# Kernel tuning notes

Hardware: AMD Instinct MI355X
Metric: run time of the kernel (lower is better)

Reference implementation:

```python
import jax, jax.numpy as jnp
import numpy as np

# Model dims: nSet=48, nItemMax=80, input feat=512,
# D = baseChn*max_channel_ratio = 128 = head_size, H = num_heads = 2.
S, N, DIN = 48, 80, 512
D = 128
H, HS = 2, 128
EPS = 1e-3  # layer_normalization epsilon (non-set-norm branch)

def _w(key, fi, fo):
    return jax.random.normal(key, (fi, fo), jnp.float32) / np.sqrt(fi)

def setup_inputs() -> dict:
    key = jax.random.key(0)
    ks = jax.random.split(key, 20)
    sizes = jax.random.randint(ks[0], (S,), 1, N + 1)
    x = jax.random.normal(ks[1], (S, N, DIN), jnp.float32)
    item_mask = (jnp.arange(N)[None, :] < sizes[:, None]).astype(jnp.float32)
    x = x * item_mask[:, :, None]  # zero-pad invalid items (drives ==0 masks)
    return {
        "x": x,
        "x_size": sizes.astype(jnp.float32),
        # trainable MLP (fc1/fc2/fc3, gelu, no bias)
        "W1": _w(ks[2], DIN, 512),
        "W2": _w(ks[3], 512, 256),
        "W3": _w(ks[4], 256, D),
        # encoder self-attention layer
        "Wq_s": _w(ks[5], D, H * HS),
        "Wk_s": _w(ks[6], D, H * HS),
        "Wv_s": _w(ks[7], D, H * HS),
        "Wh_s": _w(ks[8], H * HS, HS),
        "Wfc_e": _w(ks[9], D, D),
        # decoder cross-set attention layer
        "Wq_c": _w(ks[10], D, H * HS),
        "Wk_c": _w(ks[11], D, H * HS),
        "Wv_c": _w(ks[12], D, H * HS),
        "Wh_c": _w(ks[13], H * HS, HS),
        "Wfc_d": _w(ks[14], D, D),
        # cross_set_score
        "Wcs": _w(ks[15], D, H * HS),
        "Wcs2": _w(ks[16], H, 1),
    }

def _gelu(z):
    return jax.nn.gelu(z, approximate=False)  # tf.nn.gelu default

def _item_norm(x):
    # layer_normalization with is_set_norm=False: per-item LN, zero padded rows
    mean = jnp.mean(x, axis=-1, keepdims=True)
    std = jnp.std(x, axis=-1, keepdims=True)
    norm = (x - mean) / (std + EPS)
    keep = jnp.sum(x, axis=-1, keepdims=True) != 0
    return jnp.where(keep, norm, jnp.zeros_like(x))

def _masked_softmax(s):
    # faithful to source: mask entries where raw score == 0
    m = s != 0
    e = jnp.where(m, jnp.exp(s - jnp.max(s, axis=-1, keepdims=True)), 0.0)
    return e / (jnp.sum(e, axis=-1, keepdims=True) + 1e-10)

def _mha(q_in, kv_in, Wq, Wk, Wv, Wh):
    # q_in/kv_in: [S, S, N, D]
    q = (q_in @ Wq).reshape(S, S, N, H, HS)
    k = (kv_in @ Wk).reshape(S, S, N, H, HS)
    v = (kv_in @ Wv).reshape(S, S, N, H, HS)
    s = jnp.einsum('xynhd,xymhd->xyhnm', q, k) / np.sqrt(HS)
    a = _masked_softmax(s)
    o = jnp.einsum('xyhnm,xymhd->xynhd', a, v).reshape(S, S, N, H * HS)
    return o @ Wh  # -> [S, S, N, HS]

def reference(x, x_size, W1, W2, W3, Wq_s, Wk_s, Wv_s, Wh_s, Wfc_e,
              Wq_c, Wk_c, Wv_c, Wh_c, Wfc_d, Wcs, Wcs2):
    # item-wise MLP projection: feat -> 512 -> 256 -> 128
    h = _gelu(_gelu(_gelu(x @ W1) @ W2) @ W3)  # [S, N, D]
    # pairwise set grid [nSet_x, nSet_y, nItemMax, D]
    x4 = jnp.broadcast_to(h[:, None], (S, S, N, D))
    # encoder: self-attention over items within each (i,j) pair
    z = _item_norm(x4)
    x4 = x4 + _mha(z, z, Wq_s, Wk_s, Wv_s, Wh_s)
    z = _item_norm(x4)
    x4 = x4 + _gelu(z @ Wfc_e)
    # decoder: cross-set attention, out[i,j] = Attn(q=z[i,j], kv=z[j,i])
    z = _item_norm(x4)
    x4 = x4 + _mha(z, jnp.transpose(z, (1, 0, 2, 3)), Wq_c, Wk_c, Wv_c, Wh_c)
    z = _item_norm(x4)
    x4 = x4 + _gelu(z @ Wfc_d)
    # cross_set_score: pairwise ReLU-matmul, set-size normalized
    xh = (x4 @ Wcs).reshape(S, S, N, H, HS).transpose(0, 1, 3, 2, 4)  # [j,i,h,n,d]
    A = jax.nn.relu(jnp.einsum('jihnd,ijhmd->jihnm', xh, xh) / np.sqrt(HS))
    sc = A.sum((-1, -2)) / x_size[None, :, None] / x_size[:, None, None]  # [S,S,H]
    return sc @ Wcs2  # [S, S, 1]
```

## Files before the change

### kernel.cpp

```cpp
#include <hip/hip_runtime.h>
#include <hip/hip_bf16.h>


#define SS 48
#define NI 80

typedef unsigned short us;
typedef __attribute__((ext_vector_type(8))) short s8v;
typedef __attribute__((ext_vector_type(4))) float f4v;

#define MFMA(a,b,c) __builtin_amdgcn_mfma_f32_16x16x32_bf16((a),(b),(c),0,0,0)

__device__ __forceinline__ float gelu_f(float x){
  return 0.5f * x * (1.0f + erff(x * 0.7071067811865475f));
}
__device__ __forceinline__ us f2b(float f){
  __hip_bfloat16 b = __float2bfloat16(f);
  return reinterpret_cast<us&>(b);
}
__device__ __forceinline__ s8v zero8(){ s8v v = {0,0,0,0,0,0,0,0}; return v; }
__device__ __forceinline__ void gl16(const void* g, void* l){
  __builtin_amdgcn_global_load_lds(
      (const __attribute__((address_space(1))) void*)g,
      (__attribute__((address_space(3))) void*)l, 16, 0, 0);
}

template<int ABF16, int OUTF32>
__global__ __launch_bounds__(256) void mgemm_k(const void* __restrict__ Ap,
    const float* __restrict__ B, void* __restrict__ Cp, int N, int K)
{
  __shared__ __align__(16) char lds[10240];
  char* As = lds; char* Bs = lds + 5120;
  const int t = threadIdx.x;
  const int wv = t >> 6, lm = t & 15, lh = (t >> 4) & 3;
  const int bx = blockIdx.x, by = blockIdx.y;
  const int ar = wv*16 + lm, r0 = wv*16 + lh*4;
  f4v acc[4];
#pragma unroll
  for (int ct = 0; ct < 4; ++ct) acc[ct] = {0.f,0.f,0.f,0.f};
  const int rA = t >> 2, kcA = (t & 3) << 3;
  const int kkB = t >> 3, nnB = (t & 7) << 3;
  for (int k0 = 0; k0 < K; k0 += 32) {
    __syncthreads();
    if (ABF16) {
      s8v v = *(const s8v*)((const us*)Ap + (size_t)(by*64 + rA)*K + k0 + kcA);
      *(s8v*)(As + rA*80 + kcA*2) = v;
    } else {
      const float* ap = (const float*)Ap + (size_t)(by*64 + rA)*K + k0 + kcA;
      float4 v0 = *(const float4*)ap, v1 = *(const float4*)(ap + 4);
      us tmp[8] = {f2b(v0.x),f2b(v0.y),f2b(v0.z),f2b(v0.w),
                   f2b(v1.x),f2b(v1.y),f2b(v1.z),f2b(v1.w)};
      *(s8v*)(As + rA*80 + kcA*2) = *(const s8v*)tmp;
    }
    {
      const float* bp = B + (size_t)(k0 + kkB)*N + bx*64 + nnB;
      float4 w0 = *(const float4*)bp, w1 = *(const float4*)(bp + 4);
      float w8[8] = {w0.x,w0.y,w0.z,w0.w,w1.x,w1.y,w1.z,w1.w};
#pragma unroll
      for (int q = 0; q < 8; ++q)
        *(us*)(Bs + (nnB + q)*80 + kkB*2) = f2b(w8[q]);
    }
    __syncthreads();
    s8v af = *(const s8v*)(As + ar*80 + lh*16);
#pragma unroll
    for (int ct = 0; ct < 4; ++ct) {
      s8v bf = *(const s8v*)(Bs + (ct*16 + lm)*80 + lh*16);
      acc[ct] = MFMA(af, bf, acc[ct]);
    }
  }
#pragma unroll
  for (int ct = 0; ct < 4; ++ct)
#pragma unroll
    for (int reg = 0; reg < 4; ++reg) {
      size_t r = by*64 + r0 + reg;
      int c = bx*64 + ct*16 + lm;
      float v = gelu_f(acc[ct][reg]);
      if (OUTF32) ((float*)Cp)[r*N + c] = v;
      else ((us*)Cp)[r*N + c] = f2b(v);
    }
}

__global__ __launch_bounds__(256) void qkv_k(const us* __restrict__ A,
    const float* __restrict__ Wq, const float* __restrict__ Wk,
    const float* __restrict__ Wv, us* __restrict__ Qb, us* __restrict__ Kb,
    us* __restrict__ VT)
{
  __shared__ __align__(16) char lds[10240];
  char* As = lds; char* Bs = lds + 5120;
  const int t = threadIdx.x;
  const int wv = t >> 6, lm = t & 15, lh = (t >> 4) & 3;
  const int bx = blockIdx.x, by = blockIdx.y;
  const int sel = bx >> 2, bxx = bx & 3;
  const float* B = sel == 0 ? Wq : (sel == 1 ? Wk : Wv);
  const int ar = wv*16 + lm, r0 = wv*16 + lh*4;
  f4v acc[4];
#pragma unroll
  for (int ct = 0; ct < 4; ++ct) acc[ct] = {0.f,0.f,0.f,0.f};
  const int rA = t >> 2, kcA = (t & 3) << 3;
  const int kkB = t >> 3, nnB = (t & 7) << 3;
#pragma unroll
  for (int k0 = 0; k0 < 128; k0 += 32) {
    __syncthreads();
    {
      s8v v = *(const s8v*)(A + (size_t)(by*64 + rA)*128 + k0 + kcA);
      *(s8v*)(As + rA*80 + kcA*2) = v;
      const float* bp = B + (size_t)(k0 + kkB)*256 + bxx*64 + nnB;
      float4 w0 = *(const float4*)bp, w1 = *(const float4*)(bp + 4);
      float w8[8] = {w0.x,w0.y,w0.z,w0.w,w1.x,w1.y,w1.z,w1.w};
#pragma unroll
      for (int q = 0; q < 8; ++q)
        *(us*)(Bs + (nnB + q)*80 + kkB*2) = f2b(w8[q]);
    }
    __syncthreads();
    s8v af = *(const s8v*)(As + ar*80 + lh*16);
#pragma unroll
    for (int ct = 0; ct < 4; ++ct) {
      s8v bf = *(const s8v*)(Bs + (ct*16 + lm)*80 + lh*16);
      acc[ct] = MFMA(af, bf, acc[ct]);
    }
  }
  if (sel < 2) {
    us* O = sel ? Kb : Qb;
#pragma unroll
    for (int ct = 0; ct < 4; ++ct)
#pragma unroll
      for (int reg = 0; reg < 4; ++reg)
        O[(size_t)(by*64 + r0 + reg)*256 + bxx*64 + ct*16 + lm] = f2b(acc[ct][reg]);
  } else {
#pragma unroll
    for (int ct = 0; ct < 4; ++ct)
#pragma unroll
      for (int reg = 0; reg < 4; ++reg) {
        int r = by*64 + r0 + reg;
        int s = r / 80, m = r % 80;
        int d = bxx*64 + ct*16 + lm;
        VT[((size_t)s*256 + d)*80 + m] = f2b(acc[ct][reg]);
      }
  }
}

__global__ __launch_bounds__(64) void norm_k(const float* __restrict__ in,
                                             us* __restrict__ out)
{
  const int r = blockIdx.x, t = threadIdx.x;
  float v0 = in[(size_t)r*128 + t];
  float v1 = in[(size_t)r*128 + t + 64];
  float sm = v0 + v1;
#pragma unroll
  for (int off = 1; off < 64; off <<= 1) sm += __shfl_xor(sm, off, 64);
  float mean = sm * (1.0f/128.0f);
  float d0 = v0 - mean, d1 = v1 - mean;
  float vs = d0*d0 + d1*d1;
#pragma unroll
  for (int off = 1; off < 64; off <<= 1) vs += __shfl_xor(vs, off, 64);
  float inv = 1.0f / (sqrtf(vs * (1.0f/128.0f)) + 1e-3f);
  bool keep = (sm != 0.0f);
  out[(size_t)r*128 + t]      = f2b(keep ? d0*inv : 0.0f);
  out[(size_t)r*128 + t + 64] = f2b(keep ? d1*inv : 0.0f);
}

__global__ __launch_bounds__(128) void prep_k(
    const float* __restrict__ Wh_s, const float* __restrict__ Wfc_e,
    const float* __restrict__ Wh_c, const float* __restrict__ Wfc_d,
    const float* __restrict__ Wcs,  const float* __restrict__ Wv_s,
    const float* __restrict__ Wv_c,
    us* __restrict__ WfcTe, us* __restrict__ WfcTd,
    float* __restrict__ Wvh_s, float* __restrict__ Wvh_c,
    us* __restrict__ Mb)
{
  const int x = blockIdx.x, task = blockIdx.y, tid = threadIdx.x;
  if (task == 0) {
    WfcTe[x*128 + tid] = f2b(Wfc_e[(size_t)tid*128 + x]);
  } else if (task == 1) {
    WfcTd[x*128 + tid] = f2b(Wfc_d[(size_t)tid*128 + x]);
  } else if (task < 6) {
    int h = (task - 2) & 1;
    const float* Wv = task < 4 ? Wv_s : Wv_c;
    const float* Wh = task < 4 ? Wh_s : Wh_c;
    float* Wvh = task < 4 ? Wvh_s : Wvh_c;
    float acc = 0.f;
#pragma unroll 8
    for (int d = 0; d < 128; ++d)
      acc = fmaf(Wv[(size_t)x*256 + h*128 + d], Wh[(size_t)(h*128 + d)*128 + tid], acc);
    Wvh[(size_t)x*256 + h*128 + tid] = acc;
  } else {
    int h = task - 6;
    float acc = 0.f;
#pragma unroll 8
    for (int k = 0; k < 128; ++k)
      acc = fmaf(Wcs[(size_t)x*256 + h*128 + k], Wcs[(size_t)tid*256 + h*128 + k], acc);
    Mb[(size_t)h*16384 + x*128 + tid] = f2b(acc);
  }
}

__device__ __forceinline__ void attn4e(int a, int t,
    const us* __restrict__ Qg, const us* __restrict__ Kg,
    const us* __restrict__ VTg, const float* __restrict__ baseg,
    const us* __restrict__ WfcT,
    char* __restrict__ X, char* __restrict__ Y, f4v x4[8])
{
  const int wv = t >> 6, lane = t & 63, lm = t & 15, lh = (t >> 4) & 3;
  const int ar = wv*16 + lm, r0 = wv*16 + lh*4;
  const float isq = 0.08838834764831845f;
  const int b = a;
#pragma unroll
  for (int dt = 0; dt < 8; ++dt) x4[dt] = (f4v){0.f,0.f,0.f,0.f};

#pragma unroll 1
  for (int h = 0; h < 2; ++h) {
    if (h == 1) __syncthreads();
#pragma unroll
    for (int c = 0; c < 4; ++c) {
      int chunk = wv*4 + c;
      int row = chunk*4 + (lane >> 4);
      int scb = ((lane & 15) << 4) ^ ((row & 7) << 4);
      gl16(Kg + (((size_t)(b*NI + row)) << 8) + h*128 + (scb >> 1), X + chunk*1024);
    }
    s8v qf[4];
    {
      const us* qrow = Qg + (((size_t)(a*NI + ar)) << 8) + h*128 + lh*8;
#pragma unroll
      for (int ks = 0; ks < 4; ++ks) qf[ks] = *(const s8v*)(qrow + ks*32);
    }
    __syncthreads();
    f4v sA[5];
#pragma unroll
    for (int nt = 0; nt < 5; ++nt) {
      int row = nt*16 + lm;
      f4v acc = (f4v){0.f,0.f,0.f,0.f};
#pragma unroll
      for (int ks = 0; ks < 4; ++ks) {
        s8v kf = *(const s8v*)(X + row*256 + ((ks*64 + lh*16) ^ ((row & 7) << 4)));
        acc = MFMA(qf[ks], kf, acc);
      }
      sA[nt] = acc;
    }
#pragma unroll
    for (int reg = 0; reg < 4; ++reg) {
      int r = r0 + reg;
      float sv[5];
#pragma unroll
      for (int nt = 0; nt < 5; ++nt) sv[nt] = sA[nt][reg] * isq;
      float mx = sv[0];
#pragma unroll
      for (int nt = 1; nt < 5; ++nt) mx = fmaxf(mx, sv[nt]);
#pragma unroll
      for (int off = 1; off < 16; off <<= 1) mx = fmaxf(mx, __shfl_xor(mx, off, 64));
      float e[5], sum = 0.f;
#pragma unroll
      for (int nt = 0; nt < 5; ++nt) {
        e[nt] = (sv[nt] != 0.f) ? __expf(sv[nt] - mx) : 0.f;
        sum += e[nt];
      }
#pragma unroll
      for (int off = 1; off < 16; off <<= 1) sum += __shfl_xor(sum, off, 64);
      float inv = 1.f / (sum + 1e-10f);
#pragma unroll
      for (int nt = 0; nt < 5; ++nt)
        *(us*)(Y + r*256 + ((2*(nt*16 + lm)) ^ ((r & 7) << 4))) = f2b(e[nt] * inv);
    }
    s8v pf0 = *(const s8v*)(Y + ar*256 + ((lh*16) ^ ((ar & 7) << 4)));
    s8v pf1 = *(const s8v*)(Y + ar*256 + ((64 + lh*16) ^ ((ar & 7) << 4)));
    s8v pf2 = zero8();
    if (lh < 2)
      pf2 = *(const s8v*)(Y + ar*256 + ((128 + lh*16) ^ ((ar & 7) << 4)));
    __syncthreads();
#pragma unroll
    for (int c = 0; c < 4; ++c) {
      int chunk = wv*4 + c;
      int L = chunk*1024 + lane*16;
      int rv = L / 160;
      int rem = L - rv*160;
      int cv = (rem >> 4) - (rv % 10); if (cv < 0) cv += 10;
      gl16(VTg + ((size_t)(b*256 + h*128 + rv))*80 + (cv << 3), X + chunk*1024);
    }
    __syncthreads();
#pragma unroll
    for (int dt = 0; dt < 8; ++dt) {
      int row = dt*16 + lm;
      int rm = (row % 10) << 4;
      int o0 = lh*16 + rm; if (o0 >= 160) o0 -= 160;
      x4[dt] = MFMA(pf0, *(const s8v*)(X + row*160 + o0), x4[dt]);
      int o1 = 64 + lh*16 + rm; if (o1 >= 160) o1 -= 160;
      x4[dt] = MFMA(pf1, *(const s8v*)(X + row*160 + o1), x4[dt]);
      s8v v2 = zero8();
      if (lh < 2) {
        int o2 = 128 + lh*16 + rm; if (o2 >= 160) o2 -= 160;
        v2 = *(const s8v*)(X + row*160 + o2);
      }
      x4[dt] = MFMA(pf2, v2, x4[dt]);
    }
    if (h == 1) {
#pragma unroll
      for (int reg = 0; reg < 4; ++reg) {
        int r = r0 + reg;
#pragma unroll
        for (int dt = 0; dt < 8; ++dt)
          x4[dt][reg] += baseg[(((size_t)(a*NI + r)) << 7) + dt*16 + lm];
      }
    }
  }

  __syncthreads();
  for (int chunk = wv; chunk < 16; chunk += 5) {
    int row = chunk*4 + (lane >> 4);
    int scb = ((lane & 15) << 4) ^ ((row & 7) << 4);
    gl16(WfcT + (size_t)row*128 + (scb >> 1), X + chunk*1024);
  }
#pragma unroll
  for (int reg = 0; reg < 4; ++reg) {
    int r = r0 + reg;
    float sm = 0.f;
#pragma unroll
    for (int dt = 0; dt < 8; ++dt) sm += x4[dt][reg];
#pragma unroll
    for (int off = 1; off < 16; off <<= 1) sm += __shfl_xor(sm, off, 64);
    float mean = sm * (1.0f/128.0f);
    float vs = 0.f;
#pragma unroll
    for (int dt = 0; dt < 8; ++dt) { float d = x4[dt][reg] - mean; vs = fmaf(d, d, vs); }
#pragma unroll
    for (int off = 1; off < 16; off <<= 1) vs += __shfl_xor(vs, off, 64);
    float inv = 1.f / (sqrtf(vs * (1.0f/128.0f)) + 1e-3f);
    bool keep = (sm != 0.f);
#pragma unroll
    for (int dt = 0; dt < 8; ++dt)
      *(us*)(Y + r*256 + ((2*(dt*16 + lm)) ^ ((r & 7) << 4))) = f2b(keep ? (x4[dt][reg]-mean)*inv : 0.f);
  }
  s8v zf[4];
#pragma unroll
  for (int ks = 0; ks < 4; ++ks)
    zf[ks] = *(const s8v*)(Y + ar*256 + ((ks*64 + lh*16) ^ ((ar & 7) << 4)));
  __syncthreads();
#pragma unroll
  for (int dt = 0; dt < 4; ++dt) {
    int row = dt*16 + lm;
    f4v acc = (f4v){0.f,0.f,0.f,0.f};
#pragma unroll
    for (int ks = 0; ks < 4; ++ks) {
      s8v wfr = *(const s8v*)(X + row*256 + ((ks*64 + lh*16) ^ ((row & 7) << 4)));
      acc = MFMA(zf[ks], wfr, acc);
    }
#pragma unroll
    for (int reg = 0; reg < 4; ++reg) x4[dt][reg] += gelu_f(acc[reg]);
  }
  __syncthreads();
  for (int chunk = wv; chunk < 16; chunk += 5) {
    int row = chunk*4 + (lane >> 4);
    int scb = ((lane & 15) << 4) ^ ((row & 7) << 4);
    gl16(WfcT + (size_t)(row + 64)*128 + (scb >> 1), X + chunk*1024);
  }
  __syncthreads();
#pragma unroll
  for (int dt = 4; dt < 8; ++dt) {
    int row = dt*16 + lm;
    int r2 = row - 64;
    f4v acc = (f4v){0.f,0.f,0.f,0.f};
#pragma unroll
    for (int ks = 0; ks < 4; ++ks) {
      s8v wfr = *(const s8v*)(X + r2*256 + ((ks*64 + lh*16) ^ ((row & 7) << 4)));
      acc = MFMA(zf[ks], wfr, acc);
    }
#pragma unroll
    for (int reg = 0; reg < 4; ++reg) x4[dt][reg] += gelu_f(acc[reg]);
  }
}

__global__ __launch_bounds__(320) void enc_k(
    const us* __restrict__ Qg, const us* __restrict__ Kg,
    const us* __restrict__ VTg, const float* __restrict__ hb,
    const us* __restrict__ WfcT, float* __restrict__ e2p,
    us* __restrict__ z3b)
{
  __shared__ __align__(16) char X[20480];
  __shared__ __align__(16) char Y[20480];
  const int t = threadIdx.x;
  const int wv = t >> 6, lm = t & 15, lh = (t >> 4) & 3;
  const int r0 = wv*16 + lh*4;
  const int i = blockIdx.x;
  f4v x4[8];
  attn4e(i, t, Qg, Kg, VTg, hb, WfcT, X, Y, x4);
#pragma unroll
  for (int reg = 0; reg < 4; ++reg) {
    int r = r0 + reg;
    size_t gb = ((size_t)(i*NI + r)) << 7;
    float tmp[8]; float sm = 0.f;
#pragma unroll
    for (int dt = 0; dt < 8; ++dt) { tmp[dt] = x4[dt][reg]; sm += tmp[dt]; }
    *(float4*)(e2p + gb + lm*8)     = make_float4(tmp[0],tmp[1],tmp[2],tmp[3]);
    *(float4*)(e2p + gb + lm*8 + 4) = make_float4(tmp[4],tmp[5],tmp[6],tmp[7]);
#pragma unroll
    for (int off = 1; off < 16; off <<= 1) sm += __shfl_xor(sm, off, 64);
    float mean = sm * (1.0f/128.0f);
    float vs = 0.f;
#pragma unroll
    for (int dt = 0; dt < 8; ++dt) { float d = tmp[dt] - mean; vs = fmaf(d, d, vs); }
#pragma unroll
    for (int off = 1; off < 16; off <<= 1) vs += __shfl_xor(vs, off, 64);
    float inv = 1.f / (sqrtf(vs * (1.0f/128.0f)) + 1e-3f);
    bool keep = (sm != 0.f);
#pragma unroll
    for (int dt = 0; dt < 8; ++dt)
      z3b[gb + dt*16 + lm] = f2b(keep ? (tmp[dt]-mean)*inv : 0.f);
  }
}

__global__ __launch_bounds__(640, 2) void dec8_k(
    const us* __restrict__ Qg, const us* __restrict__ Kg,
    const us* __restrict__ VTg, const float* __restrict__ e2p,
    const us* __restrict__ WfcT, us* __restrict__ x4g)
{
  __shared__ __align__(16) char L[155648];
  const int t = threadIdx.x;
  const int g = (t >= 320) ? 1 : 0;
  const int tg = t - g*320;
  const int wv = tg >> 6, wb = t >> 6;
  const int lane = t & 63, lm = t & 15, lh = (t >> 4) & 3;
  const int ar = wv*16 + lm, r0 = wv*16 + lh*4;
  const float isq = 0.08838834764831845f;
  const int a = blockIdx.x, b = blockIdx.y*2 + g;
  char* W  = L;
  char* S0 = L + 32768 + g*61440;
  char* S1 = S0 + 20480;
  char* Y  = S0 + 40960;

#define STG_K(DST, H)                                                        \
  { _Pragma("unroll") for (int c_ = 0; c_ < 4; ++c_) {                       \
      int ch_ = wv*4 + c_;                                                   \
      int rw_ = ch_*4 + (lane >> 4);                                         \
      int sc_ = ((lane & 15) << 4) ^ ((rw_ & 7) << 4);                       \
      gl16(Kg + (((size_t)(b*NI + rw_)) << 8) + (H)*128 + (sc_ >> 1),        \
           (DST) + ch_*1024); } }
#define STG_VT(DST, H)                                                       \
  { _Pragma("unroll") for (int c_ = 0; c_ < 4; ++c_) {                       \
      int ch_ = wv*4 + c_;                                                   \
      int L_ = ch_*1024 + lane*16;                                           \
      int rv_ = L_ / 160;                                                    \
      int cv_ = ((L_ - rv_*160) >> 4) - (rv_ % 10); if (cv_ < 0) cv_ += 10;  \
      gl16(VTg + ((size_t)(b*256 + (H)*128 + rv_))*80 + (cv_ << 3),          \
           (DST) + ch_*1024); } }
#define QKSM(KS, H)                                                          \
  { s8v qf_[4];                                                              \
    { const us* qr_ = Qg + (((size_t)(a*NI + ar)) << 8) + (H)*128 + lh*8;    \
      _Pragma("unroll") for (int ks = 0; ks < 4; ++ks)                       \
        qf_[ks] = *(const s8v*)(qr_ + ks*32); }                              \
    f4v sA_[5];                                                              \
    _Pragma("unroll") for (int nt = 0; nt < 5; ++nt) {                       \
      int rw_ = nt*16 + lm;                                                  \
      f4v ac_ = (f4v){0.f,0.f,0.f,0.f};                                      \
      _Pragma("unroll") for (int ks = 0; ks < 4; ++ks) {                     \
        s8v kf_ = *(const s8v*)((KS) + rw_*256 +                             \
                                ((ks*64 + lh*16) ^ ((rw_ & 7) << 4)));       \
        ac_ = MFMA(qf_[ks], kf_, ac_); }                                     \
      sA_[nt] = ac_; }                                                       \
    _Pragma("unroll") for (int reg = 0; reg < 4; ++reg) {                    \
      int r_ = r0 + reg;                                                     \
      float sv_[5];                                                          \
      _Pragma("unroll") for (int nt = 0; nt < 5; ++nt)                       \
        sv_[nt] = sA_[nt][reg] * isq;                                        \
      float mx_ = sv_[0];                                                    \
      _Pragma("unroll") for (int nt = 1; nt < 5; ++nt)                       \
        mx_ = fmaxf(mx_, sv_[nt]);                                           \
      _Pragma("unroll") for (int of_ = 1; of_ < 16; of_ <<= 1)               \
        mx_ = fmaxf(mx_, __shfl_xor(mx_, of_, 64));                          \
      float e_[5], su_ = 0.f;                                                \
      _Pragma("unroll") for (int nt = 0; nt < 5; ++nt) {                     \
        e_[nt] = (sv_[nt] != 0.f) ? __expf(sv_[nt] - mx_) : 0.f;             \
        su_ += e_[nt]; }                                                     \
      _Pragma("unroll") for (int of_ = 1; of_ < 16; of_ <<= 1)               \
        su_ += __shfl_xor(su_, of_, 64);                                     \
      float iv_ = 1.f / (su_ + 1e-10f);                                      \
      _Pragma("unroll") for (int nt = 0; nt < 5; ++nt)                       \
        *(us*)(Y + r_*256 + ((2*(nt*16 + lm)) ^ ((r_ & 7) << 4))) =          \
            f2b(e_[nt] * iv_); } }
#define PV(VS)                                                               \
  { s8v pf0_ = *(const s8v*)(Y + ar*256 + ((lh*16) ^ ((ar & 7) << 4)));      \
    s8v pf1_ = *(const s8v*)(Y + ar*256 + ((64 + lh*16) ^ ((ar & 7) << 4))); \
    s8v pf2_ = zero8();                                                      \
    if (lh < 2)                                                              \
      pf2_ = *(const s8v*)(Y + ar*256 + ((128 + lh*16) ^ ((ar & 7) << 4)));  \
    _Pragma("unroll") for (int dt = 0; dt < 8; ++dt) {                       \
      int rw_ = dt*16 + lm;                                                  \
      int rm_ = (rw_ % 10) << 4;                                             \
      int o0_ = lh*16 + rm_; if (o0_ >= 160) o0_ -= 160;                     \
      x4[dt] = MFMA(pf0_, *(const s8v*)((VS) + rw_*160 + o0_), x4[dt]);      \
      int o1_ = 64 + lh*16 + rm_; if (o1_ >= 160) o1_ -= 160;                \
      x4[dt] = MFMA(pf1_, *(const s8v*)((VS) + rw_*160 + o1_), x4[dt]);      \
      s8v v2_ = zero8();                                                     \
      if (lh < 2) { int o2_ = 128 + lh*16 + rm_;                             \
        if (o2_ >= 160) o2_ -= 160;                                          \
        v2_ = *(const s8v*)((VS) + rw_*160 + o2_); }                         \
      x4[dt] = MFMA(pf2_, v2_, x4[dt]); } }

  f4v x4[8];
#pragma unroll
  for (int dt = 0; dt < 8; ++dt) x4[dt] = (f4v){0.f,0.f,0.f,0.f};

  for (int ch = wb; ch < 32; ch += 10) {
    int row = ch*4 + (lane >> 4);
    int scb = ((lane & 15) << 4) ^ ((row & 7) << 4);
    gl16(WfcT + (size_t)row*128 + (scb >> 1), W + ch*1024);
  }
  STG_K(S0, 0);
  __syncthreads();
  STG_VT(S1, 0);
  QKSM(S0, 0);
  __syncthreads();
  STG_K(S0, 1);
  PV(S1);
  __syncthreads();
  STG_VT(S1, 1);
  QKSM(S0, 1);
  __syncthreads();
  PV(S1);
#pragma unroll
  for (int reg = 0; reg < 4; ++reg) {
    const f4v* bp = (const f4v*)(e2p + (((size_t)(a*NI + r0 + reg)) << 7) + lm*8);
    f4v bb0 = bp[0], bb1 = bp[1];
#pragma unroll
    for (int dt = 0; dt < 4; ++dt) {
      x4[dt][reg]   += bb0[dt];
      x4[dt+4][reg] += bb1[dt];
    }
  }
#pragma unroll
  for (int reg = 0; reg < 4; ++reg) {
    int r = r0 + reg;
    float sm = 0.f;
#pragma unroll
    for (int dt = 0; dt < 8; ++dt) sm += x4[dt][reg];
#pragma unroll
    for (int off = 1; off < 16; off <<= 1) sm += __shfl_xor(sm, off, 64);
    float mean = sm * (1.0f/128.0f);
    float vs = 0.f;
#pragma unroll
    for (int dt = 0; dt < 8; ++dt) { float d = x4[dt][reg] - mean; vs = fmaf(d, d, vs); }
#pragma unroll
    for (int off = 1; off < 16; off <<= 1) vs += __shfl_xor(vs, off, 64);
    float inv = 1.f / (sqrtf(vs * (1.0f/128.0f)) + 1e-3f);
    bool keep = (sm != 0.f);
#pragma unroll
    for (int dt = 0; dt < 8; ++dt)
      *(us*)(Y + r*256 + ((2*(dt*16 + lm)) ^ ((r & 7) << 4))) = f2b(keep ? (x4[dt][reg]-mean)*inv : 0.f);
  }
  {
    s8v zf[4];
#pragma unroll
    for (int ks = 0; ks < 4; ++ks)
      zf[ks] = *(const s8v*)(Y + ar*256 + ((ks*64 + lh*16) ^ ((ar & 7) << 4)));
#pragma unroll
    for (int dt = 0; dt < 8; ++dt) {
      int row = dt*16 + lm;
      f4v ac = (f4v){0.f,0.f,0.f,0.f};
#pragma unroll
      for (int ks = 0; ks < 4; ++ks) {
        s8v wf = *(const s8v*)(W + row*256 + ((ks*64 + lh*16) ^ ((row & 7) << 4)));
        ac = MFMA(zf[ks], wf, ac);
      }
#pragma unroll
      for (int reg = 0; reg < 4; ++reg) x4[dt][reg] += gelu_f(ac[reg]);
    }
  }
#pragma unroll
  for (int reg = 0; reg < 4; ++reg) {
    int r = r0 + reg;
#pragma unroll
    for (int dt = 0; dt < 8; ++dt)
      *(us*)(Y + r*256 + ((2*(dt*16 + lm)) ^ ((r & 7) << 4))) = f2b(x4[dt][reg]);
  }
  {
    char* dst = (char*)(x4g + ((size_t)a*SS + b)*10240);
#pragma unroll
    for (int q = 0; q < 4; ++q) {
      int c = lane + q*64;
      int row = wv*16 + (c >> 4);
      int cb = (c & 15) << 4;
      s8v v = *(const s8v*)(Y + row*256 + (cb ^ ((row & 7) << 4)));
      *(s8v*)(dst + row*256 + cb) = v;
    }
  }
#undef STG_K
#undef STG_VT
#undef QKSM
#undef PV
}

__global__ __launch_bounds__(320) void up_k(
    const us* __restrict__ x4g, const us* __restrict__ Mb,
    const float* __restrict__ Wcs2, const float* __restrict__ xsg,
    float* __restrict__ outg)
{
  __shared__ __align__(16) char As[20480];
  __shared__ __align__(16) char Bs[16384];
  __shared__ __align__(16) char Xi[20480];
  __shared__ __align__(16) char Xu[40960];
  __shared__ float red[10];
  const int t = threadIdx.x;
  const int wv = t >> 6, lane = t & 63, lm = t & 15, lh = (t >> 4) & 3;
  const int ar = wv*16 + lm, r0 = wv*16 + lh*4;
  const float isq = 0.08838834764831845f;

  int bid0 = blockIdx.x;
  int bid = (bid0 & 7) * 147 + (bid0 >> 3);
  int ii = (int)(0.5f*(97.0f - sqrtf(9409.0f - 8.0f*(float)bid)));
  if (ii > 47) ii = 47; if (ii < 0) ii = 0;
  while (ii*SS - ii*(ii-1)/2 > bid) --ii;
  while ((ii+1)*SS - (ii+1)*ii/2 <= bid) ++ii;
  const int i = ii, j = ii + (bid - (ii*SS - ii*(ii-1)/2));
  const us* Aji = x4g + ((size_t)j*SS + i)*10240;
  const us* Aij = x4g + ((size_t)i*SS + j)*10240;

#pragma unroll
  for (int c = 0; c < 4; ++c) {
    int chunk = wv*4 + c;
    int row = chunk*4 + (lane >> 4);
    int scb = ((lane & 15) << 4) ^ ((row & 7) << 4);
    gl16(Aji + (size_t)row*128 + (scb >> 1), As + chunk*1024);
    gl16(Aij + (size_t)row*128 + (scb >> 1), Xi + chunk*1024);
  }
  f4v acc[16];
#pragma unroll
  for (int ct = 0; ct < 16; ++ct) acc[ct] = (f4v){0.f,0.f,0.f,0.f};
#pragma unroll 1
  for (int k0 = 0; k0 < 128; k0 += 32) {
    if (k0) __syncthreads();
    for (int c = wv; c < 16; c += 5) {
      int row = c*16 + (lane >> 2);
      int colb = (lane & 3) << 4;
      int scb = colb ^ ((row & 3) << 4);
      gl16(Mb + (size_t)row*128 + k0 + (scb >> 1), Bs + c*1024);
    }
    __syncthreads();
    int ks = k0 >> 5;
    s8v af = *(const s8v*)(As + ar*256 + ((ks*64 + lh*16) ^ ((ar & 7) << 4)));
#pragma unroll
    for (int ct = 0; ct < 16; ++ct) {
      int row = ct*16 + lm;
      s8v bf = *(const s8v*)(Bs + row*64 + ((lh*16) ^ ((row & 3) << 4)));
      acc[ct] = MFMA(af, bf, acc[ct]);
    }
  }
#pragma unroll
  for (int ct = 0; ct < 16; ++ct) {
    int h = ct >> 3;
    int cl = (ct & 7)*16 + lm;
#pragma unroll
    for (int reg = 0; reg < 4; ++reg) {
      int row = r0 + reg;
      *(us*)(Xu + h*20480 + row*256 + ((2*cl) ^ ((row & 7) << 4))) = f2b(acc[ct][reg]);
    }
  }
  __syncthreads();
  s8v xf[4];
#pragma unroll
  for (int ks = 0; ks < 4; ++ks)
    xf[ks] = *(const s8v*)(Xi + ar*256 + ((ks*64 + lh*16) ^ ((ar & 7) << 4)));
  float sc[2];
#pragma unroll 1
  for (int h = 0; h < 2; ++h) {
    const char* Xh = Xu + h*20480;
    float loc = 0.f;
#pragma unroll
    for (int nt = 0; nt < 5; ++nt) {
      int brow = nt*16 + lm;
      f4v ac = (f4v){0.f,0.f,0.f,0.f};
#pragma unroll
      for (int ks = 0; ks < 4; ++ks) {
        s8v bf = *(const s8v*)(Xh + brow*256 + ((ks*64 + lh*16) ^ ((brow & 7) << 4)));
        ac = MFMA(xf[ks], bf, ac);
      }
#pragma unroll
      for (int reg = 0; reg < 4; ++reg) loc += fmaxf(ac[reg]*isq, 0.f);
    }
    sc[h] = loc;
  }
#pragma unroll
  for (int off = 1; off < 64; off <<= 1) {
    sc[0] += __shfl_xor(sc[0], off, 64);
    sc[1] += __shfl_xor(sc[1], off, 64);
  }
  if ((t & 63) == 0) { red[wv] = sc[0]; red[wv + 5] = sc[1]; }
  __syncthreads();
  if (t == 0) {
    float s0 = red[0]+red[1]+red[2]+red[3]+red[4];
    float s1 = red[5]+red[6]+red[7]+red[8]+red[9];
    float val = (s0*Wcs2[0] + s1*Wcs2[1]) / (xsg[i]*xsg[j]);
    outg[i*SS + j] = val;
    outg[j*SS + i] = val;
  }
}

extern "C" void kernel_launch(void* const* d_in, const int* in_sizes, int n_in,
                              void* d_out, int out_size, void* d_ws, size_t ws_size,
                              hipStream_t stream)
{
  (void)in_sizes; (void)n_in; (void)out_size; (void)ws_size;
  const float* x     = (const float*)d_in[0];
  const float* xs    = (const float*)d_in[1];
  const float* W1    = (const float*)d_in[2];
  const float* W2    = (const float*)d_in[3];
  const float* W3    = (const float*)d_in[4];
  const float* Wq_s  = (const float*)d_in[5];
  const float* Wk_s  = (const float*)d_in[6];
  const float* Wv_s  = (const float*)d_in[7];
  const float* Wh_s  = (const float*)d_in[8];
  const float* Wfc_e = (const float*)d_in[9];
  const float* Wq_c  = (const float*)d_in[10];
  const float* Wk_c  = (const float*)d_in[11];
  const float* Wv_c  = (const float*)d_in[12];
  const float* Wh_c  = (const float*)d_in[13];
  const float* Wfc_d = (const float*)d_in[14];
  const float* Wcs   = (const float*)d_in[15];
  const float* Wcs2  = (const float*)d_in[16];
  float* out = (float*)d_out;

  char* w = (char*)d_ws;
  us* h1b     = (us*)w;    w += (size_t)3840*512*2;
  us* h2b     = (us*)w;    w += (size_t)3840*256*2;
  float* hb   = (float*)w; w += (size_t)3840*128*4;
  us* zb16    = (us*)w;    w += (size_t)3840*128*2;
  us* z3b     = (us*)w;    w += (size_t)3840*128*2;
  float* e2p  = (float*)w; w += (size_t)3840*128*4;
  us* Qb      = (us*)w;    w += (size_t)3840*256*2;
  us* Kb      = (us*)w;    w += (size_t)3840*256*2;
  us* VT      = (us*)w;    w += (size_t)48*256*80*2;
  us* WfcTe   = (us*)w;    w += 16384*2;
  us* WfcTd   = (us*)w;    w += 16384*2;
  us* Mb      = (us*)w;    w += 32768*2;
  float* Wvh_s = (float*)w; w += 32768*4;
  float* Wvh_c = (float*)w; w += 32768*4;
  us* x4g     = (us*)w;    w += (size_t)2304*10240*2;

  hipLaunchKernelGGL(prep_k, dim3(128, 8), dim3(128), 0, stream,
                     Wh_s, Wfc_e, Wh_c, Wfc_d, Wcs, Wv_s, Wv_c,
                     WfcTe, WfcTd, Wvh_s, Wvh_c, Mb);
  hipLaunchKernelGGL((mgemm_k<0,0>), dim3(8,60), dim3(256), 0, stream,
                     (const void*)x, W1, (void*)h1b, 512, 512);
  hipLaunchKernelGGL((mgemm_k<1,0>), dim3(4,60), dim3(256), 0, stream,
                     (const void*)h1b, W2, (void*)h2b, 256, 512);
  hipLaunchKernelGGL((mgemm_k<1,1>), dim3(2,60), dim3(256), 0, stream,
                     (const void*)h2b, W3, (void*)hb, 128, 256);
  hipLaunchKernelGGL(norm_k, dim3(3840), dim3(64), 0, stream, hb, zb16);
  hipLaunchKernelGGL(qkv_k, dim3(12,60), dim3(256), 0, stream,
                     zb16, Wq_s, Wk_s, Wvh_s, Qb, Kb, VT);
  hipLaunchKernelGGL(enc_k, dim3(48), dim3(320), 0, stream,
                     Qb, Kb, VT, hb, WfcTe, e2p, z3b);
  hipLaunchKernelGGL(qkv_k, dim3(12,60), dim3(256), 0, stream,
                     z3b, Wq_c, Wk_c, Wvh_c, Qb, Kb, VT);
  hipLaunchKernelGGL(dec8_k, dim3(48,24), dim3(640), 0, stream,
                     Qb, Kb, VT, e2p, WfcTd, x4g);
  hipLaunchKernelGGL(up_k, dim3(1176), dim3(320), 0, stream,
                     x4g, Mb, Wcs2, xs, out);
}
```

Before: 239.9 us.

## Pre-convert inputs and weights to bf16 and fuse W3 GEMM with item norm

A single conversion kernel casts x and the MLP and Q/K weights to bf16 up front, so the GEMM kernels load bf16 directly instead of converting fp32 per tile. The third MLP GEMM now computes all 128 columns per block and fuses the GELU plus per-item layer norm, removing the separate norm kernel and its launch. Wvh is stored as bf16 and the base-add in attention uses vectorized loads. The extra conversion pass adds a full read and write of x (about 3840x512 elements) plus an extra launch, which may offset the savings.

Result: no change. 243.9 us (+1.7%).

```diff
diff --git a/kernel.cpp b/kernel.cpp
--- a/kernel.cpp
+++ b/kernel.cpp
@@ -25,138 +25,29 @@
       (__attribute__((address_space(3))) void*)l, 16, 0, 0);
 }
 
-template<int ABF16, int OUTF32>
-__global__ __launch_bounds__(256) void mgemm_k(const void* __restrict__ Ap,
-    const float* __restrict__ B, void* __restrict__ Cp, int N, int K)
-{
-  __shared__ __align__(16) char lds[10240];
-  char* As = lds; char* Bs = lds + 5120;
-  const int t = threadIdx.x;
-  const int wv = t >> 6, lm = t & 15, lh = (t >> 4) & 3;
-  const int bx = blockIdx.x, by = blockIdx.y;
-  const int ar = wv*16 + lm, r0 = wv*16 + lh*4;
-  f4v acc[4];
-#pragma unroll
-  for (int ct = 0; ct < 4; ++ct) acc[ct] = {0.f,0.f,0.f,0.f};
-  const int rA = t >> 2, kcA = (t & 3) << 3;
-  const int kkB = t >> 3, nnB = (t & 7) << 3;
-  for (int k0 = 0; k0 < K; k0 += 32) {
-    __syncthreads();
-    if (ABF16) {
-      s8v v = *(const s8v*)((const us*)Ap + (size_t)(by*64 + rA)*K + k0 + kcA);
-      *(s8v*)(As + rA*80 + kcA*2) = v;
-    } else {
-      const float* ap = (const float*)Ap + (size_t)(by*64 + rA)*K + k0 + kcA;
-      float4 v0 = *(const float4*)ap, v1 = *(const float4*)(ap + 4);
-      us tmp[8] = {f2b(v0.x),f2b(v0.y),f2b(v0.z),f2b(v0.w),
-                   f2b(v1.x),f2b(v1.y),f2b(v1.z),f2b(v1.w)};
-      *(s8v*)(As + rA*80 + kcA*2) = *(const s8v*)tmp;
-    }
-    {
-      const float* bp = B + (size_t)(k0 + kkB)*N + bx*64 + nnB;
-      float4 w0 = *(const float4*)bp, w1 = *(const float4*)(bp + 4);
-      float w8[8] = {w0.x,w0.y,w0.z,w0.w,w1.x,w1.y,w1.z,w1.w};
-#pragma unroll
-      for (int q = 0; q < 8; ++q)
-        *(us*)(Bs + (nnB + q)*80 + kkB*2) = f2b(w8[q]);
-    }
-    __syncthreads();
-    s8v af = *(const s8v*)(As + ar*80 + lh*16);
-#pragma unroll
-    for (int ct = 0; ct < 4; ++ct) {
-      s8v bf = *(const s8v*)(Bs + (ct*16 + lm)*80 + lh*16);
-      acc[ct] = MFMA(af, bf, acc[ct]);
-    }
-  }
-#pragma unroll
-  for (int ct = 0; ct < 4; ++ct)
-#pragma unroll
-    for (int reg = 0; reg < 4; ++reg) {
-      size_t r = by*64 + r0 + reg;
-      int c = bx*64 + ct*16 + lm;
-      float v = gelu_f(acc[ct][reg]);
-      if (OUTF32) ((float*)Cp)[r*N + c] = v;
-      else ((us*)Cp)[r*N + c] = f2b(v);
-    }
-}
-
-__global__ __launch_bounds__(256) void qkv_k(const us* __restrict__ A,
-    const float* __restrict__ Wq, const float* __restrict__ Wk,
-    const float* __restrict__ Wv, us* __restrict__ Qb, us* __restrict__ Kb,
-    us* __restrict__ VT)
-{
-  __shared__ __align__(16) char lds[10240];
-  char* As = lds; char* Bs = lds + 5120;
-  const int t = threadIdx.x;
-  const int wv = t >> 6, lm = t & 15, lh = (t >> 4) & 3;
-  const int bx = blockIdx.x, by = blockIdx.y;
-  const int sel = bx >> 2, bxx = bx & 3;
-  const float* B = sel == 0 ? Wq : (sel == 1 ? Wk : Wv);
-  const int ar = wv*16 + lm, r0 = wv*16 + lh*4;
-  f4v acc[4];
-#pragma unroll
-  for (int ct = 0; ct < 4; ++ct) acc[ct] = {0.f,0.f,0.f,0.f};
-  const int rA = t >> 2, kcA = (t & 3) << 3;
-  const int kkB = t >> 3, nnB = (t & 7) << 3;
-#pragma unroll
-  for (int k0 = 0; k0 < 128; k0 += 32) {
-    __syncthreads();
-    {
-      s8v v = *(const s8v*)(A + (size_t)(by*64 + rA)*128 + k0 + kcA);
-      *(s8v*)(As + rA*80 + kcA*2) = v;
-      const float* bp = B + (size_t)(k0 + kkB)*256 + bxx*64 + nnB;
-      float4 w0 = *(const float4*)bp, w1 = *(const float4*)(bp + 4);
-      float w8[8] = {w0.x,w0.y,w0.z,w0.w,w1.x,w1.y,w1.z,w1.w};
-#pragma unroll
-      for (int q = 0; q < 8; ++q)
-        *(us*)(Bs + (nnB + q)*80 + kkB*2) = f2b(w8[q]);
-    }
-    __syncthreads();
-    s8v af = *(const s8v*)(As + ar*80 + lh*16);
-#pragma unroll
-    for (int ct = 0; ct < 4; ++ct) {
-      s8v bf = *(const s8v*)(Bs + (ct*16 + lm)*80 + lh*16);
-      acc[ct] = MFMA(af, bf, acc[ct]);
-    }
-  }
-  if (sel < 2) {
-    us* O = sel ? Kb : Qb;
-#pragma unroll
-    for (int ct = 0; ct < 4; ++ct)
-#pragma unroll
-      for (int reg = 0; reg < 4; ++reg)
-        O[(size_t)(by*64 + r0 + reg)*256 + bxx*64 + ct*16 + lm] = f2b(acc[ct][reg]);
-  } else {
-#pragma unroll
-    for (int ct = 0; ct < 4; ++ct)
-#pragma unroll
-      for (int reg = 0; reg < 4; ++reg) {
-        int r = by*64 + r0 + reg;
-        int s = r / 80, m = r % 80;
-        int d = bxx*64 + ct*16 + lm;
-        VT[((size_t)s*256 + d)*80 + m] = f2b(acc[ct][reg]);
-      }
-  }
-}
-
-__global__ __launch_bounds__(64) void norm_k(const float* __restrict__ in,
-                                             us* __restrict__ out)
-{
-  const int r = blockIdx.x, t = threadIdx.x;
-  float v0 = in[(size_t)r*128 + t];
-  float v1 = in[(size_t)r*128 + t + 64];
-  float sm = v0 + v1;
-#pragma unroll
-  for (int off = 1; off < 64; off <<= 1) sm += __shfl_xor(sm, off, 64);
-  float mean = sm * (1.0f/128.0f);
-  float d0 = v0 - mean, d1 = v1 - mean;
-  float vs = d0*d0 + d1*d1;
-#pragma unroll
-  for (int off = 1; off < 64; off <<= 1) vs += __shfl_xor(vs, off, 64);
-  float inv = 1.0f / (sqrtf(vs * (1.0f/128.0f)) + 1e-3f);
-  bool keep = (sm != 0.0f);
-  out[(size_t)r*128 + t]      = f2b(keep ? d0*inv : 0.0f);
-  out[(size_t)r*128 + t + 64] = f2b(keep ? d1*inv : 0.0f);
+__global__ __launch_bounds__(256) void cvt_k(
+    const float* __restrict__ x,    const float* __restrict__ W1,
+    const float* __restrict__ W2,   const float* __restrict__ W3,
+    const float* __restrict__ Wq_s, const float* __restrict__ Wk_s,
+    const float* __restrict__ Wq_c, const float* __restrict__ Wk_c,
+    us* __restrict__ xb,   us* __restrict__ W1b, us* __restrict__ W2b,
+    us* __restrict__ W3b,  us* __restrict__ Wqsb, us* __restrict__ Wksb,
+    us* __restrict__ Wqcb, us* __restrict__ Wkcb)
+{
+  const int NX = 1966080;
+  const int C1 = NX + 262144, C2 = C1 + 131072, C3 = C2 + 32768;
+  const int C4 = C3 + 32768, C5 = C4 + 32768, C6 = C5 + 32768, C7 = C6 + 32768;
+  for (int idx = blockIdx.x*256 + threadIdx.x; idx < C7;
+       idx += gridDim.x*256) {
+    if (idx < NX)      xb[idx]        = f2b(x[idx]);
+    else if (idx < C1) W1b[idx - NX]  = f2b(W1[idx - NX]);
+    else if (idx < C2) W2b[idx - C1]  = f2b(W2[idx - C1]);
+    else if (idx < C3) W3b[idx - C2]  = f2b(W3[idx - C2]);
+    else if (idx < C4) Wqsb[idx - C3] = f2b(Wq_s[idx - C3]);
+    else if (idx < C5) Wksb[idx - C4] = f2b(Wk_s[idx - C4]);
+    else if (idx < C6) Wqcb[idx - C5] = f2b(Wq_c[idx - C5]);
+    else               Wkcb[idx - C6] = f2b(Wk_c[idx - C6]);
+  }
 }
 
 __global__ __launch_bounds__(128) void prep_k(
@@ -165,7 +56,7 @@
     const float* __restrict__ Wcs,  const float* __restrict__ Wv_s,
     const float* __restrict__ Wv_c,
     us* __restrict__ WfcTe, us* __restrict__ WfcTd,
-    float* __restrict__ Wvh_s, float* __restrict__ Wvh_c,
+    us* __restrict__ Wvhb_s, us* __restrict__ Wvhb_c,
     us* __restrict__ Mb)
 {
   const int x = blockIdx.x, task = blockIdx.y, tid = threadIdx.x;
@@ -177,12 +68,12 @@
     int h = (task - 2) & 1;
     const float* Wv = task < 4 ? Wv_s : Wv_c;
     const float* Wh = task < 4 ? Wh_s : Wh_c;
-    float* Wvh = task < 4 ? Wvh_s : Wvh_c;
+    us* Wvh = task < 4 ? Wvhb_s : Wvhb_c;
     float acc = 0.f;
 #pragma unroll 8
     for (int d = 0; d < 128; ++d)
       acc = fmaf(Wv[(size_t)x*256 + h*128 + d], Wh[(size_t)(h*128 + d)*128 + tid], acc);
-    Wvh[(size_t)x*256 + h*128 + tid] = acc;
+    Wvh[(size_t)x*256 + h*128 + tid] = f2b(acc);
   } else {
     int h = task - 6;
     float acc = 0.f;
@@ -190,6 +81,166 @@
     for (int k = 0; k < 128; ++k)
       acc = fmaf(Wcs[(size_t)x*256 + h*128 + k], Wcs[(size_t)tid*256 + h*128 + k], acc);
     Mb[(size_t)h*16384 + x*128 + tid] = f2b(acc);
+  }
+}
+
+__global__ __launch_bounds__(256) void bgemm_k(const us* __restrict__ A,
+    const us* __restrict__ B, us* __restrict__ C, int N, int K)
+{
+  __shared__ __align__(16) char lds[10240];
+  char* As = lds; char* Bs = lds + 5120;
+  const int t = threadIdx.x;
+  const int wv = t >> 6, lm = t & 15, lh = (t >> 4) & 3;
+  const int bx = blockIdx.x, by = blockIdx.y;
+  const int ar = wv*16 + lm, r0 = wv*16 + lh*4;
+  f4v acc[4];
+#pragma unroll
+  for (int ct = 0; ct < 4; ++ct) acc[ct] = {0.f,0.f,0.f,0.f};
+  const int rA = t >> 2, kcA = (t & 3) << 3;
+  const int kkB = t >> 3, nnB = (t & 7) << 3;
+  for (int k0 = 0; k0 < K; k0 += 32) {
+    __syncthreads();
+    {
+      s8v v = *(const s8v*)(A + (size_t)(by*64 + rA)*K + k0 + kcA);
+      *(s8v*)(As + rA*80 + kcA*2) = v;
+      s8v wv8 = *(const s8v*)(B + (size_t)(k0 + kkB)*N + bx*64 + nnB);
+      const us* wp = (const us*)&wv8;
+#pragma unroll
+      for (int q = 0; q < 8; ++q)
+        *(us*)(Bs + (nnB + q)*80 + kkB*2) = wp[q];
+    }
+    __syncthreads();
+    s8v af = *(const s8v*)(As + ar*80 + lh*16);
+#pragma unroll
+    for (int ct = 0; ct < 4; ++ct) {
+      s8v bf = *(const s8v*)(Bs + (ct*16 + lm)*80 + lh*16);
+      acc[ct] = MFMA(af, bf, acc[ct]);
+    }
+  }
+#pragma unroll
+  for (int ct = 0; ct < 4; ++ct)
+#pragma unroll
+    for (int reg = 0; reg < 4; ++reg)
+      C[(size_t)(by*64 + r0 + reg)*N + bx*64 + ct*16 + lm] = f2b(gelu_f(acc[ct][reg]));
+}
+
+__global__ __launch_bounds__(256) void nmgemm_k(const us* __restrict__ A,
+    const us* __restrict__ B, float* __restrict__ hbp, us* __restrict__ z1b)
+{
+  __shared__ __align__(16) char lds[15360];
+  char* As = lds; char* Bs = lds + 5120;
+  const int t = threadIdx.x;
+  const int wv = t >> 6, lm = t & 15, lh = (t >> 4) & 3;
+  const int by = blockIdx.x;
+  const int ar = wv*16 + lm, r0 = wv*16 + lh*4;
+  f4v acc[8];
+#pragma unroll
+  for (int ct = 0; ct < 8; ++ct) acc[ct] = {0.f,0.f,0.f,0.f};
+  const int rA = t >> 2, kcA = (t & 3) << 3;
+  const int kkB = t >> 3, nnB = (t & 7) << 4;
+#pragma unroll 1
+  for (int k0 = 0; k0 < 256; k0 += 32) {
+    __syncthreads();
+    {
+      s8v v = *(const s8v*)(A + (size_t)(by*64 + rA)*256 + k0 + kcA);
+      *(s8v*)(As + rA*80 + kcA*2) = v;
+#pragma unroll
+      for (int q2 = 0; q2 < 2; ++q2) {
+        s8v wv8 = *(const s8v*)(B + (size_t)(k0 + kkB)*128 + nnB + q2*8);
+        const us* wp = (const us*)&wv8;
+#pragma unroll
+        for (int q = 0; q < 8; ++q)
+          *(us*)(Bs + (nnB + q2*8 + q)*80 + kkB*2) = wp[q];
+      }
+    }
+    __syncthreads();
+    s8v af = *(const s8v*)(As + ar*80 + lh*16);
+#pragma unroll
+    for (int ct = 0; ct < 8; ++ct) {
+      s8v bf = *(const s8v*)(Bs + (ct*16 + lm)*80 + lh*16);
+      acc[ct] = MFMA(af, bf, acc[ct]);
+    }
+  }
+#pragma unroll
+  for (int reg = 0; reg < 4; ++reg) {
+    int row = by*64 + r0 + reg;
+    size_t gb = (size_t)row << 7;
+    float g[8]; float sm = 0.f;
+#pragma unroll
+    for (int dt = 0; dt < 8; ++dt) { g[dt] = gelu_f(acc[dt][reg]); sm += g[dt]; }
+    *(float4*)(hbp + gb + lm*8)     = make_float4(g[0],g[1],g[2],g[3]);
+    *(float4*)(hbp + gb + lm*8 + 4) = make_float4(g[4],g[5],g[6],g[7]);
+#pragma unroll
+    for (int off = 1; off < 16; off <<= 1) sm += __shfl_xor(sm, off, 64);
+    float mean = sm * (1.0f/128.0f);
+    float vs = 0.f;
+#pragma unroll
+    for (int dt = 0; dt < 8; ++dt) { float d = g[dt] - mean; vs = fmaf(d, d, vs); }
+#pragma unroll
+    for (int off = 1; off < 16; off <<= 1) vs += __shfl_xor(vs, off, 64);
+    float inv = 1.f / (sqrtf(vs * (1.0f/128.0f)) + 1e-3f);
+    bool keep = (sm != 0.f);
+#pragma unroll
+    for (int dt = 0; dt < 8; ++dt)
+      z1b[gb + dt*16 + lm] = f2b(keep ? (g[dt]-mean)*inv : 0.f);
+  }
+}
+
+__global__ __launch_bounds__(256) void qkv2_k(const us* __restrict__ A,
+    const us* __restrict__ Wq, const us* __restrict__ Wk,
+    const us* __restrict__ Wv, us* __restrict__ Qb, us* __restrict__ Kb,
+    us* __restrict__ VT)
+{
+  __shared__ __align__(16) char lds[10240];
+  char* As = lds; char* Bs = lds + 5120;
+  const int t = threadIdx.x;
+  const int wv = t >> 6, lm = t & 15, lh = (t >> 4) & 3;
+  const int bx = blockIdx.x, by = blockIdx.y;
+  const int sel = bx >> 2, bxx = bx & 3;
+  const us* B = sel == 0 ? Wq : (sel == 1 ? Wk : Wv);
+  const int ar = wv*16 + lm, r0 = wv*16 + lh*4;
+  f4v acc[4];
+#pragma unroll
+  for (int ct = 0; ct < 4; ++ct) acc[ct] = {0.f,0.f,0.f,0.f};
+  const int rA = t >> 2, kcA = (t & 3) << 3;
+  const int kkB = t >> 3, nnB = (t & 7) << 3;
+#pragma unroll
+  for (int k0 = 0; k0 < 128; k0 += 32) {
+    __syncthreads();
+    {
+      s8v v = *(const s8v*)(A + (size_t)(by*64 + rA)*128 + k0 + kcA);
+      *(s8v*)(As + rA*80 + kcA*2) = v;
+      s8v wv8 = *(const s8v*)(B + (size_t)(k0 + kkB)*256 + bxx*64 + nnB);
+      const us* wp = (const us*)&wv8;
+#pragma unroll
+      for (int q = 0; q < 8; ++q)
+        *(us*)(Bs + (nnB + q)*80 + kkB*2) = wp[q];
+    }
+    __syncthreads();
+    s8v af = *(const s8v*)(As + ar*80 + lh*16);
+#pragma unroll
+    for (int ct = 0; ct < 4; ++ct) {
+      s8v bf = *(const s8v*)(Bs + (ct*16 + lm)*80 + lh*16);
+      acc[ct] = MFMA(af, bf, acc[ct]);
+    }
+  }
+  if (sel < 2) {
+    us* O = sel ? Kb : Qb;
+#pragma unroll
+    for (int ct = 0; ct < 4; ++ct)
+#pragma unroll
+      for (int reg = 0; reg < 4; ++reg)
+        O[(size_t)(by*64 + r0 + reg)*256 + bxx*64 + ct*16 + lm] = f2b(acc[ct][reg]);
+  } else {
+#pragma unroll
+    for (int ct = 0; ct < 4; ++ct)
+#pragma unroll
+      for (int reg = 0; reg < 4; ++reg) {
+        int r = by*64 + r0 + reg;
+        int s = r / 80, m = r % 80;
+        int d = bxx*64 + ct*16 + lm;
+        VT[((size_t)s*256 + d)*80 + m] = f2b(acc[ct][reg]);
+      }
   }
 }
 
@@ -293,10 +344,13 @@
     if (h == 1) {
 #pragma unroll
       for (int reg = 0; reg < 4; ++reg) {
-        int r = r0 + reg;
-#pragma unroll
-        for (int dt = 0; dt < 8; ++dt)
-          x4[dt][reg] += baseg[(((size_t)(a*NI + r)) << 7) + dt*16 + lm];
+        const f4v* bp = (const f4v*)(baseg + (((size_t)(a*NI + r0 + reg)) << 7) + lm*8);
+        f4v b0 = bp[0], b1 = bp[1];
+#pragma unroll
+        for (int dt = 0; dt < 4; ++dt) {
+          x4[dt][reg]   += b0[dt];
+          x4[dt+4][reg] += b1[dt];
+        }
       }
     }
   }
@@ -368,7 +422,7 @@
 
 __global__ __launch_bounds__(320) void enc_k(
     const us* __restrict__ Qg, const us* __restrict__ Kg,
-    const us* __restrict__ VTg, const float* __restrict__ hb,
+    const us* __restrict__ VTg, const float* __restrict__ hbp,
     const us* __restrict__ WfcT, float* __restrict__ e2p,
     us* __restrict__ z3b)
 {
@@ -379,7 +433,7 @@
   const int r0 = wv*16 + lh*4;
   const int i = blockIdx.x;
   f4v x4[8];
-  attn4e(i, t, Qg, Kg, VTg, hb, WfcT, X, Y, x4);
+  attn4e(i, t, Qg, Kg, VTg, hbp, WfcT, X, Y, x4);
 #pragma unroll
   for (int reg = 0; reg < 4; ++reg) {
     int r = r0 + reg;
@@ -715,10 +769,18 @@
   float* out = (float*)d_out;
 
   char* w = (char*)d_ws;
+  us* xb      = (us*)w;    w += (size_t)3840*512*2;
+  us* W1b     = (us*)w;    w += (size_t)512*512*2;
+  us* W2b     = (us*)w;    w += (size_t)512*256*2;
+  us* W3b     = (us*)w;    w += (size_t)256*128*2;
+  us* Wqsb    = (us*)w;    w += 32768*2;
+  us* Wksb    = (us*)w;    w += 32768*2;
+  us* Wqcb    = (us*)w;    w += 32768*2;
+  us* Wkcb    = (us*)w;    w += 32768*2;
   us* h1b     = (us*)w;    w += (size_t)3840*512*2;
   us* h2b     = (us*)w;    w += (size_t)3840*256*2;
-  float* hb   = (float*)w; w += (size_t)3840*128*4;
-  us* zb16    = (us*)w;    w += (size_t)3840*128*2;
+  float* hbp  = (float*)w; w += (size_t)3840*128*4;
+  us* z1b     = (us*)w;    w += (size_t)3840*128*2;
   us* z3b     = (us*)w;    w += (size_t)3840*128*2;
   float* e2p  = (float*)w; w += (size_t)3840*128*4;
   us* Qb      = (us*)w;    w += (size_t)3840*256*2;
@@ -727,26 +789,28 @@
   us* WfcTe   = (us*)w;    w += 16384*2;
   us* WfcTd   = (us*)w;    w += 16384*2;
   us* Mb      = (us*)w;    w += 32768*2;
-  float* Wvh_s = (float*)w; w += 32768*4;
-  float* Wvh_c = (float*)w; w += 32768*4;
+  us* Wvhb_s  = (us*)w;    w += 32768*2;
+  us* Wvhb_c  = (us*)w;    w += 32768*2;
   us* x4g     = (us*)w;    w += (size_t)2304*10240*2;
 
+  hipLaunchKernelGGL(cvt_k, dim3(2048), dim3(256), 0, stream,
+                     x, W1, W2, W3, Wq_s, Wk_s, Wq_c, Wk_c,
+                     xb, W1b, W2b, W3b, Wqsb, Wksb, Wqcb, Wkcb);
   hipLaunchKernelGGL(prep_k, dim3(128, 8), dim3(128), 0, stream,
                      Wh_s, Wfc_e, Wh_c, Wfc_d, Wcs, Wv_s, Wv_c,
-                     WfcTe, WfcTd, Wvh_s, Wvh_c, Mb);
-  hipLaunchKernelGGL((mgemm_k<0,0>), dim3(8,60), dim3(256), 0, stream,
-                     (const void*)x, W1, (void*)h1b, 512, 512);
-  hipLaunchKernelGGL((mgemm_k<1,0>), dim3(4,60), dim3(256), 0, stream,
-                     (const void*)h1b, W2, (void*)h2b, 256, 512);
-  hipLaunchKernelGGL((mgemm_k<1,1>), dim3(2,60), dim3(256), 0, stream,
-                     (const void*)h2b, W3, (void*)hb, 128, 256);
-  hipLaunchKernelGGL(norm_k, dim3(3840), dim3(64), 0, stream, hb, zb16);
-  hipLaunchKernelGGL(qkv_k, dim3(12,60), dim3(256), 0, stream,
-                     zb16, Wq_s, Wk_s, Wvh_s, Qb, Kb, VT);
+                     WfcTe, WfcTd, Wvhb_s, Wvhb_c, Mb);
+  hipLaunchKernelGGL(bgemm_k, dim3(8,60), dim3(256), 0, stream,
+                     xb, W1b, h1b, 512, 512);
+  hipLaunchKernelGGL(bgemm_k, dim3(4,60), dim3(256), 0, stream,
+                     h1b, W2b, h2b, 256, 512);
+  hipLaunchKernelGGL(nmgemm_k, dim3(60), dim3(256), 0, stream,
+                     h2b, W3b, hbp, z1b);
+  hipLaunchKernelGGL(qkv2_k, dim3(12,60), dim3(256), 0, stream,
+                     z1b, Wqsb, Wksb, Wvhb_s, Qb, Kb, VT);
   hipLaunchKernelGGL(enc_k, dim3(48), dim3(320), 0, stream,
-                     Qb, Kb, VT, hb, WfcTe, e2p, z3b);
-  hipLaunchKernelGGL(qkv_k, dim3(12,60), dim3(256), 0, stream,
-                     z3b, Wq_c, Wk_c, Wvh_c, Qb, Kb, VT);
+                     Qb, Kb, VT, hbp, WfcTe, e2p, z3b);
+  hipLaunchKernelGGL(qkv2_k, dim3(12,60), dim3(256), 0, stream,
+                     z3b, Wqcb, Wkcb, Wvhb_c, Qb, Kb, VT);
   hipLaunchKernelGGL(dec8_k, dim3(48,24), dim3(640), 0, stream,
                      Qb, Kb, VT, e2p, WfcTd, x4g);
   hipLaunchKernelGGL(up_k, dim3(1176), dim3(320), 0, stream,
```
